# Kernel optimization log

Hardware: AMD Instinct MI355X
Metric: run time of the kernel (lower is better)

## Reference

```python
import jax, jax.numpy as jnp
import numpy as np

B, IN, E, H, V, MAX_LEN = 512, 64, 512, 1024, 1024, 32
LN_EPS = 1e-5


def setup_inputs() -> dict:
    key = jax.random.key(0)
    ks = jax.random.split(key, 16)
    s = 0.02
    n = lambda k, shp: jax.random.normal(k, shp, jnp.float32) * s
    return {
        "x": jax.random.normal(ks[0], (B, IN), jnp.float32),
        "w_in": n(ks[1], (E, IN)), "b_in": jnp.zeros((E,), jnp.float32),
        "w_ih0": n(ks[2], (4 * H, E)), "w_hh0": n(ks[3], (4 * H, H)),
        "b_ih0": jnp.zeros((4 * H,), jnp.float32), "b_hh0": jnp.zeros((4 * H,), jnp.float32),
        "w_ih1": n(ks[4], (4 * H, H)), "w_hh1": n(ks[5], (4 * H, H)),
        "b_ih1": jnp.zeros((4 * H,), jnp.float32), "b_hh1": jnp.zeros((4 * H,), jnp.float32),
        "ln_g": jnp.ones((H,), jnp.float32), "ln_b": jnp.zeros((H,), jnp.float32),
        "w_out": n(ks[6], (V, H)), "b_out": jnp.zeros((V,), jnp.float32),
        "emb": n(ks[7], (V, E)),
    }


def _lstm_cell(x, h, c, w_ih, w_hh, b_ih, b_hh):
    # PyTorch LSTMCell: gates ordered (input, forget, cell, output)
    gates = x @ w_ih.T + h @ w_hh.T + b_ih + b_hh  # [B, 4H]
    i, f, g, o = jnp.split(gates, 4, axis=1)
    i, f, o = jax.nn.sigmoid(i), jax.nn.sigmoid(f), jax.nn.sigmoid(o)
    g = jnp.tanh(g)
    c2 = f * c + i * g
    h2 = o * jnp.tanh(c2)
    return h2, c2


def reference(x, w_in, b_in, w_ih0, w_hh0, b_ih0, b_hh0,
              w_ih1, w_hh1, b_ih1, b_hh1, ln_g, ln_b, w_out, b_out, emb):
    bsz = x.shape[0]
    hid = w_hh0.shape[1]
    inp = x @ w_in.T + b_in  # [B, E]
    z = jnp.zeros((bsz, hid), jnp.float32)
    init = (z, z, z, z, inp)

    def step(carry, _):
        h0, c0, h1, c1, cur = carry
        h0, c0 = _lstm_cell(cur, h0, c0, w_ih0, w_hh0, b_ih0, b_hh0)
        h1, c1 = _lstm_cell(h0, h1, c1, w_ih1, w_hh1, b_ih1, b_hh1)
        mu = jnp.mean(h1, axis=-1, keepdims=True)
        var = jnp.mean((h1 - mu) ** 2, axis=-1, keepdims=True)
        hn = (h1 - mu) / jnp.sqrt(var + LN_EPS) * ln_g + ln_b
        lp = jax.nn.log_softmax(hn @ w_out.T + b_out, axis=-1)  # [B, V]
        ent = -jnp.sum(jnp.exp(lp) * lp, axis=-1)  # [B]
        sym = jnp.argmax(lp, axis=-1)  # eval-mode (deterministic) path
        logprob = jnp.take_along_axis(lp, sym[:, None], axis=1)[:, 0]
        nxt = emb[sym]  # [B, E]
        return (h0, c0, h1, c1, nxt), (sym, logprob, ent)

    _, (seq, logits, ent) = jax.lax.scan(step, init, None, length=MAX_LEN)
    seq, logits, ent = seq.T, logits.T, ent.T  # [B, MAX_LEN]
    zcol_f = jnp.zeros((bsz, 1), jnp.float32)
    zcol_i = jnp.zeros((bsz, 1), seq.dtype)
    seq = jnp.concatenate([seq, zcol_i], axis=1)
    logits = jnp.concatenate([logits, zcol_f], axis=1)
    ent = jnp.concatenate([ent, zcol_f], axis=1)
    return seq, logits, ent
```

## Files before the change

kernel.cpp:

```cpp
#include <hip/hip_runtime.h>
#include <hip/hip_bf16.h>
#include <math.h>

#define BQ   512
#define EDIM 512
#define HDIM 1024
#define VDIM 1024
#define TLEN 32
#define TOUT 33
#define PLS  (BQ * VDIM)

typedef _Float16 half8  __attribute__((ext_vector_type(8)));
typedef _Float16 half4v __attribute__((ext_vector_type(4)));
typedef float    f32x16 __attribute__((ext_vector_type(16)));

#define GLOAD_LDS16(gp, lp) __builtin_amdgcn_global_load_lds( \
    (const __attribute__((address_space(1))) void*)(gp),      \
    (__attribute__((address_space(3))) void*)(lp), 16, 0, 0)

__device__ __forceinline__ size_t packoff(int r, int k, int K) {
    return (size_t)(r >> 5) * (size_t)(32 * K) + (size_t)(k >> 4) * 512
         + (size_t)((k >> 3) & 1) * 256 + (size_t)(r & 31) * 8 + (size_t)(k & 7);
}

__device__ _Float16 g_curh[BQ*EDIM], g_curl[BQ*EDIM];
__device__ _Float16 g_h0h[BQ*HDIM], g_h0l[BQ*HDIM];
__device__ _Float16 g_h1h[BQ*HDIM], g_h1l[BQ*HDIM];
__device__ _Float16 g_hnh[BQ*HDIM], g_hnl[BQ*HDIM];
__device__ float    g_c0[BQ*HDIM], g_c1[BQ*HDIM];

__device__ _Float16 g_wih0h[4*HDIM*EDIM], g_wih0l[4*HDIM*EDIM];
__device__ _Float16 g_whh0h[4*HDIM*HDIM], g_whh0l[4*HDIM*HDIM];
__device__ _Float16 g_wih1h[4*HDIM*HDIM], g_wih1l[4*HDIM*HDIM];
__device__ _Float16 g_whh1h[4*HDIM*HDIM], g_whh1l[4*HDIM*HDIM];
__device__ _Float16 g_wouth[VDIM*HDIM],   g_woutl[VDIM*HDIM];

__device__ float g_gates[BQ * 4 * HDIM];
__device__ float g_part_lg[4 * PLS];
__device__ float g_bsum0[4*HDIM], g_bsum1[4*HDIM];

__global__ void init_kernel(float* __restrict__ out,
                            const float* __restrict__ bi0, const float* __restrict__ bh0,
                            const float* __restrict__ bi1, const float* __restrict__ bh1) {
    int i = blockIdx.x * 256 + threadIdx.x;
    g_c0[i] = 0.f; g_c1[i] = 0.f;
    g_h0h[i] = (_Float16)0.f; g_h0l[i] = (_Float16)0.f;
    g_h1h[i] = (_Float16)0.f; g_h1l[i] = (_Float16)0.f;
    if (i < 4 * HDIM) {
        g_bsum0[i] = bi0[i] + bh0[i];
        g_bsum1[i] = bi1[i] + bh1[i];
    }
    if (i < 3 * BQ) {
        int which = i / BQ, b = i % BQ;
        out[(size_t)which * BQ * TOUT + (size_t)b * TOUT + (TOUT - 1)] = 0.f;
    }
}

__global__ void split_pack_kernel(const float* __restrict__ w, _Float16* __restrict__ hi,
                                  _Float16* __restrict__ lo, int klog, int nquads) {
    int q = blockIdx.x * 256 + threadIdx.x;
    if (q >= nquads) return;
    int e = q * 4;
    int r = e >> klog, k = e & ((1 << klog) - 1);
    float4 v = ((const float4*)w)[q];
    half4v h, l;
    h[0] = (_Float16)v.x; l[0] = (_Float16)((v.x - (float)h[0]) * 4096.f);
    h[1] = (_Float16)v.y; l[1] = (_Float16)((v.y - (float)h[1]) * 4096.f);
    h[2] = (_Float16)v.z; l[2] = (_Float16)((v.z - (float)h[2]) * 4096.f);
    h[3] = (_Float16)v.w; l[3] = (_Float16)((v.w - (float)h[3]) * 4096.f);
    size_t po = packoff(r, k, 1 << klog);
    *(half4v*)&hi[po] = h;
    *(half4v*)&lo[po] = l;
}

__device__ __forceinline__ void split1(float x, _Float16* hp, _Float16* lp) {
    _Float16 h = (_Float16)x;
    *hp = h;
    *lp = (_Float16)((x - (float)h) * 4096.f);
}

__global__ __launch_bounds__(256) void gemm_pipe(
    const _Float16* __restrict__ Ah1, const _Float16* __restrict__ Al1, int K1,
    const _Float16* __restrict__ Wh1, const _Float16* __restrict__ Wl1,
    const _Float16* __restrict__ Ah2, const _Float16* __restrict__ Al2, int K2,
    const _Float16* __restrict__ Wh2, const _Float16* __restrict__ Wl2,
    const float* __restrict__ bias, float* __restrict__ outp,
    int N, int S, int NTP)
{
    __shared__ __align__(16) _Float16 sA[4][2][2][2][512];
    int tid = threadIdx.x;
    int l = tid & 63, w = tid >> 6;
    int lr = l & 31, lq = l >> 5;
    int plw = w >> 1, mhw = w & 1;

    int wb = blockIdx.x;
    int xcd = wb & 7, q = wb >> 3;
    int nt = xcd * NTP + q % NTP;
    int rest = q / NTP;
    int s = rest % S;
    int mb = rest / S;

    int kch1 = K1 / S, kch2 = (K2 > 0) ? (K2 / S) : 0;
    int n1 = kch1 >> 5;
    int nit = n1 + (kch2 >> 5);

    const _Float16* pA1 = (plw ? Al1 : Ah1)
        + (size_t)(mb*2 + mhw) * (size_t)(32*K1) + (size_t)((s*kch1) >> 4) * 512 + (size_t)l*8;
    const _Float16* pWh1 = Wh1
        + (size_t)(nt*4 + w) * (size_t)(32*K1) + (size_t)((s*kch1) >> 4) * 512 + (size_t)l*8;
    const _Float16* pWl1 = Wl1
        + (size_t)(nt*4 + w) * (size_t)(32*K1) + (size_t)((s*kch1) >> 4) * 512 + (size_t)l*8;
    const _Float16 *pA2 = pA1, *pWh2 = pWh1, *pWl2 = pWl1;
    if (K2 > 0) {
        pA2 = (plw ? Al2 : Ah2)
            + (size_t)(mb*2 + mhw) * (size_t)(32*K2) + (size_t)((s*kch2) >> 4) * 512 + (size_t)l*8;
        pWh2 = Wh2
            + (size_t)(nt*4 + w) * (size_t)(32*K2) + (size_t)((s*kch2) >> 4) * 512 + (size_t)l*8;
        pWl2 = Wl2
            + (size_t)(nt*4 + w) * (size_t)(32*K2) + (size_t)((s*kch2) >> 4) * 512 + (size_t)l*8;
    }

    f32x16 accM0 = {}, accM1 = {}, accL0 = {}, accL1 = {};
    half8 B0h[2], B0l[2], B1h[2], B1l[2], B2h[2], B2l[2], B3h[2], B3l[2];

#define STAGE(IT, SLOT, BH, BL)                                                \
    {                                                                          \
        int it_ = (IT);                                                        \
        bool g1_ = it_ < n1;                                                   \
        const _Float16* ap_ = g1_ ? pA1 : pA2;                                 \
        const _Float16* wh_ = g1_ ? pWh1 : pWh2;                               \
        const _Float16* wl_ = g1_ ? pWl1 : pWl2;                               \
        size_t off_ = (size_t)(g1_ ? it_ : it_ - n1) * 1024;                   \
        GLOAD_LDS16(ap_ + off_,       &sA[SLOT][plw][mhw][0][0]);              \
        GLOAD_LDS16(ap_ + off_ + 512, &sA[SLOT][plw][mhw][1][0]);              \
        BH[0] = *(const half8*)(wh_ + off_);                                   \
        BH[1] = *(const half8*)(wh_ + off_ + 512);                             \
        BL[0] = *(const half8*)(wl_ + off_);                                   \
        BL[1] = *(const half8*)(wl_ + off_ + 512);                             \
    }

#define COMPUTE(BUF, BH, BL)                                                   \
    {                                                                          \
        _Pragma("unroll")                                                      \
        for (int kh_ = 0; kh_ < 2; ++kh_) {                                    \
            half8 ah0 = *(const half8*)&sA[BUF][0][0][kh_][(size_t)l * 8];     \
            half8 ah1 = *(const half8*)&sA[BUF][0][1][kh_][(size_t)l * 8];     \
            half8 al0 = *(const half8*)&sA[BUF][1][0][kh_][(size_t)l * 8];     \
            half8 al1 = *(const half8*)&sA[BUF][1][1][kh_][(size_t)l * 8];     \
            accM0 = __builtin_amdgcn_mfma_f32_32x32x16_f16(ah0, BH[kh_], accM0, 0, 0, 0); \
            accM1 = __builtin_amdgcn_mfma_f32_32x32x16_f16(ah1, BH[kh_], accM1, 0, 0, 0); \
            accL0 = __builtin_amdgcn_mfma_f32_32x32x16_f16(ah0, BL[kh_], accL0, 0, 0, 0); \
            accL1 = __builtin_amdgcn_mfma_f32_32x32x16_f16(ah1, BL[kh_], accL1, 0, 0, 0); \
            accL0 = __builtin_amdgcn_mfma_f32_32x32x16_f16(al0, BH[kh_], accL0, 0, 0, 0); \
            accL1 = __builtin_amdgcn_mfma_f32_32x32x16_f16(al1, BH[kh_], accL1, 0, 0, 0); \
        }                                                                      \
    }

#define WAITSYNC(IT)                                                           \
    {                                                                          \
        if ((IT) < nit - 2)      asm volatile("s_waitcnt vmcnt(12)" ::: "memory"); \
        else if ((IT) == nit - 2) asm volatile("s_waitcnt vmcnt(6)"  ::: "memory"); \
        else                      asm volatile("s_waitcnt vmcnt(0)"  ::: "memory"); \
        __builtin_amdgcn_sched_barrier(0);                                     \
        __builtin_amdgcn_s_barrier();                                          \
    }

#define ITER(IT, BUF, BHc, BLc, BHn, BLn)                                      \
    {                                                                          \
        if ((IT) + 2 < nit) STAGE((IT) + 2, ((BUF) + 2) & 3, BHn, BLn);        \
        WAITSYNC(IT);                                                          \
        COMPUTE(BUF, BHc, BLc);                                                \
    }

    STAGE(0, 0, B0h, B0l);
    STAGE(1, 1, B1h, B1l);

    for (int base = 0; base < nit; base += 4) {
        ITER(base + 0, 0, B0h, B0l, B2h, B2l);
        ITER(base + 1, 1, B1h, B1l, B3h, B3l);
        ITER(base + 2, 2, B2h, B2l, B0h, B0l);
        ITER(base + 3, 3, B3h, B3l, B1h, B1l);
    }
#undef ITER
#undef WAITSYNC
#undef COMPUTE
#undef STAGE

    int n = nt * 128 + w * 32 + lr;
    int m0 = mb * 64;
    float bv = bias ? bias[n] : 0.f;
    float* op = outp + (size_t)s * BQ * N;
    #pragma unroll
    for (int r = 0; r < 16; ++r) {
        int row = (r & 3) + 8 * (r >> 2) + 4 * lq;
        op[(size_t)(m0 + row) * N + n]      = accM0[r] + accL0[r] * (1.f / 4096.f) + bv;
        op[(size_t)(m0 + 32 + row) * N + n] = accM1[r] + accL1[r] * (1.f / 4096.f) + bv;
    }
}

#define GBK 16
#define GPAD 68
__global__ __launch_bounds__(256) void gemm_in(const float* __restrict__ x,
                                               const float* __restrict__ w_in,
                                               const float* __restrict__ b_in) {
    __shared__ __align__(16) float As[GBK][GPAD];
    __shared__ __align__(16) float Bs[GBK][GPAD];
    int tid = threadIdx.x;
    int tx = tid & 15, ty = tid >> 4;
    int m0 = blockIdx.y * 64, n0 = blockIdx.x * 64;
    int lm = tid >> 2, lk = (tid & 3) << 2;
    const int K = 64;
    float acc[4][4] = {};
    for (int k0 = 0; k0 < K; k0 += GBK) {
        float4 av = *(const float4*)(x + (size_t)(m0 + lm) * K + k0 + lk);
        float4 wv = *(const float4*)(w_in + (size_t)(n0 + lm) * K + k0 + lk);
        As[lk + 0][lm] = av.x; As[lk + 1][lm] = av.y;
        As[lk + 2][lm] = av.z; As[lk + 3][lm] = av.w;
        Bs[lk + 0][lm] = wv.x; Bs[lk + 1][lm] = wv.y;
        Bs[lk + 2][lm] = wv.z; Bs[lk + 3][lm] = wv.w;
        __syncthreads();
        #pragma unroll
        for (int kk = 0; kk < GBK; ++kk) {
            float4 a  = *(const float4*)&As[kk][ty * 4];
            float4 bq = *(const float4*)&Bs[kk][tx * 4];
            float aa[4] = {a.x, a.y, a.z, a.w};
            float bb[4] = {bq.x, bq.y, bq.z, bq.w};
            #pragma unroll
            for (int i = 0; i < 4; ++i)
                #pragma unroll
                for (int j = 0; j < 4; ++j)
                    acc[i][j] = fmaf(aa[i], bb[j], acc[i][j]);
        }
        __syncthreads();
    }
    #pragma unroll
    for (int i = 0; i < 4; ++i) {
        int m = m0 + ty * 4 + i;
        int n = n0 + tx * 4;
        half4v h, lo;
        #pragma unroll
        for (int j = 0; j < 4; ++j) {
            float v = acc[i][j] + b_in[n + j];
            _Float16 hv = (_Float16)v;
            h[j] = hv;
            lo[j] = (_Float16)((v - (float)hv) * 4096.f);
        }
        size_t po = packoff(m, n, EDIM);
        *(half4v*)&g_curh[po] = h;
        *(half4v*)&g_curl[po] = lo;
    }
}

__device__ __forceinline__ float sigm(float x) { return 1.f / (1.f + expf(-x)); }

__global__ void lstm0_kernel() {
    int qidx = blockIdx.x * 256 + threadIdx.x;
    int b = qidx >> 8;
    int j = (qidx & 255) * 4;
    size_t base = (size_t)b * 4096;
    float4 G[4];
    #pragma unroll
    for (int g = 0; g < 4; ++g) G[g] = *(const float4*)&g_gates[base + g * 1024 + j];
    size_t hb = (size_t)b * HDIM + j;
    float4 cin = *(const float4*)&g_c0[hb];
    float ci[4] = {cin.x, cin.y, cin.z, cin.w};
    float gi[4] = {G[0].x, G[0].y, G[0].z, G[0].w};
    float gf[4] = {G[1].x, G[1].y, G[1].z, G[1].w};
    float gg[4] = {G[2].x, G[2].y, G[2].z, G[2].w};
    float go[4] = {G[3].x, G[3].y, G[3].z, G[3].w};
    float c[4], h[4];
    half4v hh, hl;
    #pragma unroll
    for (int r = 0; r < 4; ++r) {
        c[r] = sigm(gf[r]) * ci[r] + sigm(gi[r]) * tanhf(gg[r]);
        h[r] = sigm(go[r]) * tanhf(c[r]);
        _Float16 hi16 = (_Float16)h[r];
        hh[r] = hi16;
        hl[r] = (_Float16)((h[r] - (float)hi16) * 4096.f);
    }
    *(float4*)&g_c0[hb] = {c[0], c[1], c[2], c[3]};
    size_t po = packoff(b, j, HDIM);
    *(half4v*)&g_h0h[po] = hh;
    *(half4v*)&g_h0l[po] = hl;
}

__global__ __launch_bounds__(256) void lstm1_ln_kernel(
    const float* __restrict__ ln_g, const float* __restrict__ ln_b)
{
    __shared__ float sbuf[4];
    int b = blockIdx.x, tid = threadIdx.x;
    int lane = tid & 63, wid = tid >> 6;
    int j = tid * 4;
    size_t base = (size_t)b * 4096;
    float4 G[4];
    #pragma unroll
    for (int g = 0; g < 4; ++g) G[g] = *(const float4*)&g_gates[base + g * 1024 + j];
    size_t hb = (size_t)b * HDIM + j;
    float4 cin = *(const float4*)&g_c1[hb];
    float ci[4] = {cin.x, cin.y, cin.z, cin.w};
    float gi[4] = {G[0].x, G[0].y, G[0].z, G[0].w};
    float gf[4] = {G[1].x, G[1].y, G[1].z, G[1].w};
    float gg[4] = {G[2].x, G[2].y, G[2].z, G[2].w};
    float go[4] = {G[3].x, G[3].y, G[3].z, G[3].w};
    float c[4], h[4];
    float sum = 0.f;
    #pragma unroll
    for (int r = 0; r < 4; ++r) {
        c[r] = sigm(gf[r]) * ci[r] + sigm(gi[r]) * tanhf(gg[r]);
        h[r] = sigm(go[r]) * tanhf(c[r]);
        sum += h[r];
    }
    *(float4*)&g_c1[hb] = {c[0], c[1], c[2], c[3]};
    size_t po = packoff(b, j, HDIM);
    half4v h1h, h1l;
    #pragma unroll
    for (int r = 0; r < 4; ++r) {
        _Float16 hi16 = (_Float16)h[r];
        h1h[r] = hi16;
        h1l[r] = (_Float16)((h[r] - (float)hi16) * 4096.f);
    }
    *(half4v*)&g_h1h[po] = h1h;
    *(half4v*)&g_h1l[po] = h1l;

    for (int off = 32; off > 0; off >>= 1) sum += __shfl_down(sum, off, 64);
    if (lane == 0) sbuf[wid] = sum;
    __syncthreads();
    float mu = (sbuf[0] + sbuf[1] + sbuf[2] + sbuf[3]) * (1.f / HDIM);
    __syncthreads();
    float sq = 0.f;
    #pragma unroll
    for (int r = 0; r < 4; ++r) { float d = h[r] - mu; sq += d * d; }
    for (int off = 32; off > 0; off >>= 1) sq += __shfl_down(sq, off, 64);
    if (lane == 0) sbuf[wid] = sq;
    __syncthreads();
    float var = (sbuf[0] + sbuf[1] + sbuf[2] + sbuf[3]) * (1.f / HDIM);
    float rstd = 1.f / sqrtf(var + 1e-5f);
    half4v nh, nl;
    #pragma unroll
    for (int r = 0; r < 4; ++r) {
        float hn = (h[r] - mu) * rstd * ln_g[j + r] + ln_b[j + r];
        _Float16 hi16 = (_Float16)hn;
        nh[r] = hi16;
        nl[r] = (_Float16)((hn - (float)hi16) * 4096.f);
    }
    *(half4v*)&g_hnh[po] = nh;
    *(half4v*)&g_hnl[po] = nl;
}

__global__ __launch_bounds__(256) void softmax_row_kernel(
    const float* __restrict__ b_out, const float* __restrict__ emb,
    float* __restrict__ out, int t)
{
    __shared__ float swv[4];
    __shared__ int   swi[4];
    __shared__ float sZ[4], sS[4];
    __shared__ float s_max;
    __shared__ int   s_idx;
    int b = blockIdx.x, tid = threadIdx.x;
    int lane = tid & 63, wid = tid >> 6;
    size_t base = (size_t)b * VDIM + 4 * tid;
    float4 xv = *(const float4*)&b_out[4 * tid];
    #pragma unroll
    for (int s = 0; s < 4; ++s) {
        float4 p = *(const float4*)&g_part_lg[(size_t)s * PLS + base];
        xv.x += p.x; xv.y += p.y; xv.z += p.z; xv.w += p.w;
    }

    float mv = xv.x; int mi = 4 * tid;
    if (xv.y > mv) { mv = xv.y; mi = 4 * tid + 1; }
    if (xv.z > mv) { mv = xv.z; mi = 4 * tid + 2; }
    if (xv.w > mv) { mv = xv.w; mi = 4 * tid + 3; }
    for (int off = 32; off > 0; off >>= 1) {
        float ov = __shfl_down(mv, off, 64);
        int   oi = __shfl_down(mi, off, 64);
        if (ov > mv || (ov == mv && oi < mi)) { mv = ov; mi = oi; }
    }
    if (lane == 0) { swv[wid] = mv; swi[wid] = mi; }
    __syncthreads();
    if (tid == 0) {
        mv = swv[0]; mi = swi[0];
        for (int w = 1; w < 4; ++w)
            if (swv[w] > mv || (swv[w] == mv && swi[w] < mi)) { mv = swv[w]; mi = swi[w]; }
        s_max = mv; s_idx = mi;
    }
    __syncthreads();
    float xmax = s_max;

    float sv[4] = {xv.x - xmax, xv.y - xmax, xv.z - xmax, xv.w - xmax};
    float z = 0.f, s1 = 0.f;
    #pragma unroll
    for (int r = 0; r < 4; ++r) { float e = expf(sv[r]); z += e; s1 += e * sv[r]; }
    for (int off = 32; off > 0; off >>= 1) {
        z  += __shfl_down(z, off, 64);
        s1 += __shfl_down(s1, off, 64);
    }
    if (lane == 0) { sZ[wid] = z; sS[wid] = s1; }
    __syncthreads();
    if (tid == 0) {
        float Z = sZ[0] + sZ[1] + sZ[2] + sZ[3];
        float S1 = sS[0] + sS[1] + sS[2] + sS[3];
        float logZ = logf(Z);
        float ent = logZ - S1 / Z;
        out[(size_t)b * TOUT + t]                         = (float)s_idx;
        out[(size_t)BQ * TOUT + (size_t)b * TOUT + t]     = -logZ;
        out[(size_t)2 * BQ * TOUT + (size_t)b * TOUT + t] = ent;
    }
    __syncthreads();
    int sym = s_idx;
    const float* e = emb + (size_t)sym * EDIM;
    for (int j = tid; j < EDIM; j += 256) {
        size_t po = packoff(b, j, EDIM);
        split1(e[j], &g_curh[po], &g_curl[po]);
    }
}

extern "C" void kernel_launch(void* const* d_in, const int* in_sizes, int n_in,
                              void* d_out, int out_size, void* d_ws, size_t ws_size,
                              hipStream_t stream) {
    const float* x     = (const float*)d_in[0];
    const float* w_in  = (const float*)d_in[1];
    const float* b_in  = (const float*)d_in[2];
    const float* w_ih0 = (const float*)d_in[3];
    const float* w_hh0 = (const float*)d_in[4];
    const float* b_ih0 = (const float*)d_in[5];
    const float* b_hh0 = (const float*)d_in[6];
    const float* w_ih1 = (const float*)d_in[7];
    const float* w_hh1 = (const float*)d_in[8];
    const float* b_ih1 = (const float*)d_in[9];
    const float* b_hh1 = (const float*)d_in[10];
    const float* ln_g  = (const float*)d_in[11];
    const float* ln_b  = (const float*)d_in[12];
    const float* w_out = (const float*)d_in[13];
    const float* b_out = (const float*)d_in[14];
    const float* emb   = (const float*)d_in[15];
    float* out = (float*)d_out;

    _Float16 *wih0h, *wih0l, *whh0h, *whh0l, *wih1h, *wih1l, *whh1h, *whh1l, *wouth, *woutl;
    hipGetSymbolAddress((void**)&wih0h, HIP_SYMBOL(g_wih0h));
    hipGetSymbolAddress((void**)&wih0l, HIP_SYMBOL(g_wih0l));
    hipGetSymbolAddress((void**)&whh0h, HIP_SYMBOL(g_whh0h));
    hipGetSymbolAddress((void**)&whh0l, HIP_SYMBOL(g_whh0l));
    hipGetSymbolAddress((void**)&wih1h, HIP_SYMBOL(g_wih1h));
    hipGetSymbolAddress((void**)&wih1l, HIP_SYMBOL(g_wih1l));
    hipGetSymbolAddress((void**)&whh1h, HIP_SYMBOL(g_whh1h));
    hipGetSymbolAddress((void**)&whh1l, HIP_SYMBOL(g_whh1l));
    hipGetSymbolAddress((void**)&wouth, HIP_SYMBOL(g_wouth));
    hipGetSymbolAddress((void**)&woutl, HIP_SYMBOL(g_woutl));
    _Float16 *curh, *curl, *h0h, *h0l, *h1h, *h1l, *hnh, *hnl;
    hipGetSymbolAddress((void**)&curh, HIP_SYMBOL(g_curh));
    hipGetSymbolAddress((void**)&curl, HIP_SYMBOL(g_curl));
    hipGetSymbolAddress((void**)&h0h, HIP_SYMBOL(g_h0h));
    hipGetSymbolAddress((void**)&h0l, HIP_SYMBOL(g_h0l));
    hipGetSymbolAddress((void**)&h1h, HIP_SYMBOL(g_h1h));
    hipGetSymbolAddress((void**)&h1l, HIP_SYMBOL(g_h1l));
    hipGetSymbolAddress((void**)&hnh, HIP_SYMBOL(g_hnh));
    hipGetSymbolAddress((void**)&hnl, HIP_SYMBOL(g_hnl));
    float *gates, *part_lg, *bsum0, *bsum1;
    hipGetSymbolAddress((void**)&gates, HIP_SYMBOL(g_gates));
    hipGetSymbolAddress((void**)&part_lg, HIP_SYMBOL(g_part_lg));
    hipGetSymbolAddress((void**)&bsum0, HIP_SYMBOL(g_bsum0));
    hipGetSymbolAddress((void**)&bsum1, HIP_SYMBOL(g_bsum1));

    init_kernel<<<(BQ * HDIM) / 256, 256, 0, stream>>>(out, b_ih0, b_hh0, b_ih1, b_hh1);

    split_pack_kernel<<<(4*HDIM*EDIM/4 + 255)/256, 256, 0, stream>>>(w_ih0, wih0h, wih0l, 9,  4*HDIM*EDIM/4);
    split_pack_kernel<<<(4*HDIM*HDIM/4 + 255)/256, 256, 0, stream>>>(w_hh0, whh0h, whh0l, 10, 4*HDIM*HDIM/4);
    split_pack_kernel<<<(4*HDIM*HDIM/4 + 255)/256, 256, 0, stream>>>(w_ih1, wih1h, wih1l, 10, 4*HDIM*HDIM/4);
    split_pack_kernel<<<(4*HDIM*HDIM/4 + 255)/256, 256, 0, stream>>>(w_hh1, whh1h, whh1l, 10, 4*HDIM*HDIM/4);
    split_pack_kernel<<<(VDIM*HDIM/4 + 255)/256, 256, 0, stream>>>(w_out, wouth, woutl, 10, VDIM*HDIM/4);

    gemm_in<<<dim3(EDIM / 64, BQ / 64), 256, 0, stream>>>(x, w_in, b_in);

    for (int t = 0; t < TLEN; ++t) {
        gemm_pipe<<<256, 256, 0, stream>>>(
            curh, curl, EDIM, wih0h, wih0l,
            h0h, h0l, HDIM, whh0h, whh0l,
            bsum0, gates, 4 * HDIM, 1, 4);
        lstm0_kernel<<<(BQ * HDIM / 4) / 256, 256, 0, stream>>>();

        gemm_pipe<<<256, 256, 0, stream>>>(
            h0h, h0l, HDIM, wih1h, wih1l,
            h1h, h1l, HDIM, whh1h, whh1l,
            bsum1, gates, 4 * HDIM, 1, 4);
        lstm1_ln_kernel<<<BQ, 256, 0, stream>>>(ln_g, ln_b);

        gemm_pipe<<<256, 256, 0, stream>>>(
            hnh, hnl, HDIM, wouth, woutl,
            (const _Float16*)nullptr, (const _Float16*)nullptr, 0,
            (const _Float16*)nullptr, (const _Float16*)nullptr,
            (const float*)nullptr, part_lg, VDIM, 4, 1);

        softmax_row_kernel<<<BQ, 256, 0, stream>>>(b_out, emb, out, t);
    }
}
```

Before: 3.127 ms.

## Enlarge GEMM tile to 128x128 with LDS-staged weights and split-K partials

```diff
diff --git a/kernel.cpp b/kernel.cpp
--- a/kernel.cpp
+++ b/kernel.cpp
@@ -8,6 +8,7 @@
 #define VDIM 1024
 #define TLEN 32
 #define TOUT 33
+#define PGS  (BQ * 4 * HDIM)
 #define PLS  (BQ * VDIM)
 
 typedef _Float16 half8  __attribute__((ext_vector_type(8)));
@@ -35,8 +36,8 @@
 __device__ _Float16 g_whh1h[4*HDIM*HDIM], g_whh1l[4*HDIM*HDIM];
 __device__ _Float16 g_wouth[VDIM*HDIM],   g_woutl[VDIM*HDIM];
 
-__device__ float g_gates[BQ * 4 * HDIM];
-__device__ float g_part_lg[4 * PLS];
+__device__ float g_part_g[2 * PGS];
+__device__ float g_part_lg[8 * PLS];
 __device__ float g_bsum0[4*HDIM], g_bsum1[4*HDIM];
 
 __global__ void init_kernel(float* __restrict__ out,
@@ -79,7 +80,7 @@
     *lp = (_Float16)((x - (float)h) * 4096.f);
 }
 
-__global__ __launch_bounds__(256) void gemm_pipe(
+__global__ __launch_bounds__(512, 2) void gemm_big(
     const _Float16* __restrict__ Ah1, const _Float16* __restrict__ Al1, int K1,
     const _Float16* __restrict__ Wh1, const _Float16* __restrict__ Wl1,
     const _Float16* __restrict__ Ah2, const _Float16* __restrict__ Al2, int K2,
@@ -87,11 +88,12 @@
     const float* __restrict__ bias, float* __restrict__ outp,
     int N, int S, int NTP)
 {
-    __shared__ __align__(16) _Float16 sA[4][2][2][2][512];
+    __shared__ __align__(16) _Float16 sA[4][2][4][2][512];
+    __shared__ __align__(16) _Float16 sB[4][2][4][2][512];
     int tid = threadIdx.x;
     int l = tid & 63, w = tid >> 6;
     int lr = l & 31, lq = l >> 5;
-    int plw = w >> 1, mhw = w & 1;
+    int mw = w >> 2, nw = w & 3;
 
     int wb = blockIdx.x;
     int xcd = wb & 7, q = wb >> 3;
@@ -104,90 +106,93 @@
     int n1 = kch1 >> 5;
     int nit = n1 + (kch2 >> 5);
 
-    const _Float16* pA1 = (plw ? Al1 : Ah1)
-        + (size_t)(mb*2 + mhw) * (size_t)(32*K1) + (size_t)((s*kch1) >> 4) * 512 + (size_t)l*8;
-    const _Float16* pWh1 = Wh1
-        + (size_t)(nt*4 + w) * (size_t)(32*K1) + (size_t)((s*kch1) >> 4) * 512 + (size_t)l*8;
-    const _Float16* pWl1 = Wl1
-        + (size_t)(nt*4 + w) * (size_t)(32*K1) + (size_t)((s*kch1) >> 4) * 512 + (size_t)l*8;
-    const _Float16 *pA2 = pA1, *pWh2 = pWh1, *pWl2 = pWl1;
-    if (K2 > 0) {
-        pA2 = (plw ? Al2 : Ah2)
-            + (size_t)(mb*2 + mhw) * (size_t)(32*K2) + (size_t)((s*kch2) >> 4) * 512 + (size_t)l*8;
-        pWh2 = Wh2
-            + (size_t)(nt*4 + w) * (size_t)(32*K2) + (size_t)((s*kch2) >> 4) * 512 + (size_t)l*8;
-        pWl2 = Wl2
-            + (size_t)(nt*4 + w) * (size_t)(32*K2) + (size_t)((s*kch2) >> 4) * 512 + (size_t)l*8;
+    const _Float16* fsrc1[4];
+    const _Float16* fsrc2[4];
+    _Float16* fdst0[4];
+    #pragma unroll
+    for (int qq = 0; qq < 4; ++qq) {
+        int fq = w * 4 + qq;
+        bool isA = fq < 16;
+        int r_ = isA ? fq : fq - 16;
+        int pl = r_ >> 3, idx = (r_ >> 1) & 3, kh = r_ & 1;
+        int strip = isA ? (mb * 4 + idx) : (nt * 4 + idx);
+        const _Float16* p1 = isA ? (pl ? Al1 : Ah1) : (pl ? Wl1 : Wh1);
+        fsrc1[qq] = p1 + (size_t)strip * (size_t)(32 * K1)
+                  + (size_t)((s * kch1) >> 4) * 512 + (size_t)kh * 512 + (size_t)l * 8;
+        if (K2 > 0) {
+            const _Float16* p2 = isA ? (pl ? Al2 : Ah2) : (pl ? Wl2 : Wh2);
+            fsrc2[qq] = p2 + (size_t)strip * (size_t)(32 * K2)
+                      + (size_t)((s * kch2) >> 4) * 512 + (size_t)kh * 512 + (size_t)l * 8;
+        } else {
+            fsrc2[qq] = fsrc1[qq];
+        }
+        fdst0[qq] = isA ? &sA[0][pl][idx][kh][0] : &sB[0][pl][idx][kh][0];
     }
 
     f32x16 accM0 = {}, accM1 = {}, accL0 = {}, accL1 = {};
-    half8 B0h[2], B0l[2], B1h[2], B1l[2], B2h[2], B2l[2], B3h[2], B3l[2];
-
-#define STAGE(IT, SLOT, BH, BL)                                                \
+
+#define STAGE(IT, SLOT)                                                        \
     {                                                                          \
         int it_ = (IT);                                                        \
         bool g1_ = it_ < n1;                                                   \
-        const _Float16* ap_ = g1_ ? pA1 : pA2;                                 \
-        const _Float16* wh_ = g1_ ? pWh1 : pWh2;                               \
-        const _Float16* wl_ = g1_ ? pWl1 : pWl2;                               \
         size_t off_ = (size_t)(g1_ ? it_ : it_ - n1) * 1024;                   \
-        GLOAD_LDS16(ap_ + off_,       &sA[SLOT][plw][mhw][0][0]);              \
-        GLOAD_LDS16(ap_ + off_ + 512, &sA[SLOT][plw][mhw][1][0]);              \
-        BH[0] = *(const half8*)(wh_ + off_);                                   \
-        BH[1] = *(const half8*)(wh_ + off_ + 512);                             \
-        BL[0] = *(const half8*)(wl_ + off_);                                   \
-        BL[1] = *(const half8*)(wl_ + off_ + 512);                             \
-    }
-
-#define COMPUTE(BUF, BH, BL)                                                   \
+        _Pragma("unroll")                                                      \
+        for (int qq = 0; qq < 4; ++qq) {                                       \
+            const _Float16* sp_ = (g1_ ? fsrc1[qq] : fsrc2[qq]) + off_;        \
+            GLOAD_LDS16(sp_, fdst0[qq] + (size_t)(SLOT) * 8192);               \
+        }                                                                      \
+    }
+
+#define COMPUTE(BUF)                                                           \
     {                                                                          \
         _Pragma("unroll")                                                      \
         for (int kh_ = 0; kh_ < 2; ++kh_) {                                    \
-            half8 ah0 = *(const half8*)&sA[BUF][0][0][kh_][(size_t)l * 8];     \
-            half8 ah1 = *(const half8*)&sA[BUF][0][1][kh_][(size_t)l * 8];     \
-            half8 al0 = *(const half8*)&sA[BUF][1][0][kh_][(size_t)l * 8];     \
-            half8 al1 = *(const half8*)&sA[BUF][1][1][kh_][(size_t)l * 8];     \
-            accM0 = __builtin_amdgcn_mfma_f32_32x32x16_f16(ah0, BH[kh_], accM0, 0, 0, 0); \
-            accM1 = __builtin_amdgcn_mfma_f32_32x32x16_f16(ah1, BH[kh_], accM1, 0, 0, 0); \
-            accL0 = __builtin_amdgcn_mfma_f32_32x32x16_f16(ah0, BL[kh_], accL0, 0, 0, 0); \
-            accL1 = __builtin_amdgcn_mfma_f32_32x32x16_f16(ah1, BL[kh_], accL1, 0, 0, 0); \
-            accL0 = __builtin_amdgcn_mfma_f32_32x32x16_f16(al0, BH[kh_], accL0, 0, 0, 0); \
-            accL1 = __builtin_amdgcn_mfma_f32_32x32x16_f16(al1, BH[kh_], accL1, 0, 0, 0); \
+            half8 ah0 = *(const half8*)&sA[BUF][0][2*mw  ][kh_][(size_t)l * 8];\
+            half8 ah1 = *(const half8*)&sA[BUF][0][2*mw+1][kh_][(size_t)l * 8];\
+            half8 al0 = *(const half8*)&sA[BUF][1][2*mw  ][kh_][(size_t)l * 8];\
+            half8 al1 = *(const half8*)&sA[BUF][1][2*mw+1][kh_][(size_t)l * 8];\
+            half8 bh  = *(const half8*)&sB[BUF][0][nw][kh_][(size_t)l * 8];    \
+            half8 bl  = *(const half8*)&sB[BUF][1][nw][kh_][(size_t)l * 8];    \
+            accM0 = __builtin_amdgcn_mfma_f32_32x32x16_f16(ah0, bh, accM0, 0, 0, 0); \
+            accM1 = __builtin_amdgcn_mfma_f32_32x32x16_f16(ah1, bh, accM1, 0, 0, 0); \
+            accL0 = __builtin_amdgcn_mfma_f32_32x32x16_f16(ah0, bl, accL0, 0, 0, 0); \
+            accL1 = __builtin_amdgcn_mfma_f32_32x32x16_f16(ah1, bl, accL1, 0, 0, 0); \
+            accL0 = __builtin_amdgcn_mfma_f32_32x32x16_f16(al0, bh, accL0, 0, 0, 0); \
+            accL1 = __builtin_amdgcn_mfma_f32_32x32x16_f16(al1, bh, accL1, 0, 0, 0); \
         }                                                                      \
     }
 
 #define WAITSYNC(IT)                                                           \
     {                                                                          \
-        if ((IT) < nit - 2)      asm volatile("s_waitcnt vmcnt(12)" ::: "memory"); \
-        else if ((IT) == nit - 2) asm volatile("s_waitcnt vmcnt(6)"  ::: "memory"); \
-        else                      asm volatile("s_waitcnt vmcnt(0)"  ::: "memory"); \
+        if ((IT) < nit - 2)       asm volatile("s_waitcnt vmcnt(8)" ::: "memory"); \
+        else if ((IT) == nit - 2) asm volatile("s_waitcnt vmcnt(4)" ::: "memory"); \
+        else                      asm volatile("s_waitcnt vmcnt(0)" ::: "memory"); \
         __builtin_amdgcn_sched_barrier(0);                                     \
         __builtin_amdgcn_s_barrier();                                          \
     }
 
-#define ITER(IT, BUF, BHc, BLc, BHn, BLn)                                      \
+#define ITER(IT, BUF)                                                          \
     {                                                                          \
-        if ((IT) + 2 < nit) STAGE((IT) + 2, ((BUF) + 2) & 3, BHn, BLn);        \
+        if ((IT) + 2 < nit) STAGE((IT) + 2, ((BUF) + 2) & 3);                  \
         WAITSYNC(IT);                                                          \
-        COMPUTE(BUF, BHc, BLc);                                                \
-    }
-
-    STAGE(0, 0, B0h, B0l);
-    STAGE(1, 1, B1h, B1l);
-
+        COMPUTE(BUF);                                                          \
+    }
+
+    STAGE(0, 0);
+    STAGE(1, 1);
     for (int base = 0; base < nit; base += 4) {
-        ITER(base + 0, 0, B0h, B0l, B2h, B2l);
-        ITER(base + 1, 1, B1h, B1l, B3h, B3l);
-        ITER(base + 2, 2, B2h, B2l, B0h, B0l);
-        ITER(base + 3, 3, B3h, B3l, B1h, B1l);
+        ITER(base + 0, 0);
+        ITER(base + 1, 1);
+        ITER(base + 2, 2);
+        ITER(base + 3, 3);
     }
 #undef ITER
 #undef WAITSYNC
 #undef COMPUTE
 #undef STAGE
 
-    int n = nt * 128 + w * 32 + lr;
-    int m0 = mb * 64;
+    int n = nt * 128 + nw * 32 + lr;
+    int m0 = mb * 128 + mw * 64;
     float bv = bias ? bias[n] : 0.f;
     float* op = outp + (size_t)s * BQ * N;
     #pragma unroll
@@ -260,7 +265,15 @@
     size_t base = (size_t)b * 4096;
     float4 G[4];
     #pragma unroll
-    for (int g = 0; g < 4; ++g) G[g] = *(const float4*)&g_gates[base + g * 1024 + j];
+    for (int g = 0; g < 4; ++g) {
+        float4 p0 = *(const float4*)&g_part_g[base + g * 1024 + j];
+        float4 p1 = *(const float4*)&g_part_g[PGS + base + g * 1024 + j];
+        float4 bs = *(const float4*)&g_bsum0[g * 1024 + j];
+        G[g].x = p0.x + p1.x + bs.x;
+        G[g].y = p0.y + p1.y + bs.y;
+        G[g].z = p0.z + p1.z + bs.z;
+        G[g].w = p0.w + p1.w + bs.w;
+    }
     size_t hb = (size_t)b * HDIM + j;
     float4 cin = *(const float4*)&g_c0[hb];
     float ci[4] = {cin.x, cin.y, cin.z, cin.w};
@@ -294,7 +307,15 @@
     size_t base = (size_t)b * 4096;
     float4 G[4];
     #pragma unroll
-    for (int g = 0; g < 4; ++g) G[g] = *(const float4*)&g_gates[base + g * 1024 + j];
+    for (int g = 0; g < 4; ++g) {
+        float4 p0 = *(const float4*)&g_part_g[base + g * 1024 + j];
+        float4 p1 = *(const float4*)&g_part_g[PGS + base + g * 1024 + j];
+        float4 bs = *(const float4*)&g_bsum1[g * 1024 + j];
+        G[g].x = p0.x + p1.x + bs.x;
+        G[g].y = p0.y + p1.y + bs.y;
+        G[g].z = p0.z + p1.z + bs.z;
+        G[g].w = p0.w + p1.w + bs.w;
+    }
     size_t hb = (size_t)b * HDIM + j;
     float4 cin = *(const float4*)&g_c1[hb];
     float ci[4] = {cin.x, cin.y, cin.z, cin.w};
@@ -361,7 +382,7 @@
     size_t base = (size_t)b * VDIM + 4 * tid;
     float4 xv = *(const float4*)&b_out[4 * tid];
     #pragma unroll
-    for (int s = 0; s < 4; ++s) {
+    for (int s = 0; s < 8; ++s) {
         float4 p = *(const float4*)&g_part_lg[(size_t)s * PLS + base];
         xv.x += p.x; xv.y += p.y; xv.z += p.z; xv.w += p.w;
     }
@@ -455,11 +476,9 @@
     hipGetSymbolAddress((void**)&h1l, HIP_SYMBOL(g_h1l));
     hipGetSymbolAddress((void**)&hnh, HIP_SYMBOL(g_hnh));
     hipGetSymbolAddress((void**)&hnl, HIP_SYMBOL(g_hnl));
-    float *gates, *part_lg, *bsum0, *bsum1;
-    hipGetSymbolAddress((void**)&gates, HIP_SYMBOL(g_gates));
+    float *part_g, *part_lg;
+    hipGetSymbolAddress((void**)&part_g, HIP_SYMBOL(g_part_g));
     hipGetSymbolAddress((void**)&part_lg, HIP_SYMBOL(g_part_lg));
-    hipGetSymbolAddress((void**)&bsum0, HIP_SYMBOL(g_bsum0));
-    hipGetSymbolAddress((void**)&bsum1, HIP_SYMBOL(g_bsum1));
 
     init_kernel<<<(BQ * HDIM) / 256, 256, 0, stream>>>(out, b_ih0, b_hh0, b_ih1, b_hh1);
 
@@ -472,23 +491,23 @@
     gemm_in<<<dim3(EDIM / 64, BQ / 64), 256, 0, stream>>>(x, w_in, b_in);
 
     for (int t = 0; t < TLEN; ++t) {
-        gemm_pipe<<<256, 256, 0, stream>>>(
+        gemm_big<<<256, 512, 0, stream>>>(
             curh, curl, EDIM, wih0h, wih0l,
             h0h, h0l, HDIM, whh0h, whh0l,
-            bsum0, gates, 4 * HDIM, 1, 4);
+            (const float*)nullptr, part_g, 4 * HDIM, 2, 4);
         lstm0_kernel<<<(BQ * HDIM / 4) / 256, 256, 0, stream>>>();
 
-        gemm_pipe<<<256, 256, 0, stream>>>(
+        gemm_big<<<256, 512, 0, stream>>>(
             h0h, h0l, HDIM, wih1h, wih1l,
             h1h, h1l, HDIM, whh1h, whh1l,
-            bsum1, gates, 4 * HDIM, 1, 4);
+            (const float*)nullptr, part_g, 4 * HDIM, 2, 4);
         lstm1_ln_kernel<<<BQ, 256, 0, stream>>>(ln_g, ln_b);
 
-        gemm_pipe<<<256, 256, 0, stream>>>(
+        gemm_big<<<256, 512, 0, stream>>>(
             hnh, hnl, HDIM, wouth, woutl,
             (const _Float16*)nullptr, (const _Float16*)nullptr, 0,
             (const _Float16*)nullptr, (const _Float16*)nullptr,
-            (const float*)nullptr, part_lg, VDIM, 4, 1);
+            (const float*)nullptr, part_lg, VDIM, 8, 1);
 
         softmax_row_kernel<<<BQ, 256, 0, stream>>>(b_out, emb, out, t);
     }
```

After: 2.842 ms. -9.1%, faster.
